# Kernel optimization log

Hardware: AMD Instinct MI355X
Metric: run time of the kernel (lower is better)

Reference implementation:

```python
import jax, jax.numpy as jnp
import numpy as np

N = 25000        # nodes
E = 400000       # edges (avg 16 neighbors)
C1 = 8           # output_size (scalar channels into TP)
COUT = 16        # channels_out
LMAX = 2
NB = 8           # number_of_basis
RMAX = 5.0       # max_radius
EMB = 16         # atom embedding dim
NATOM = 10
WNUM = (LMAX + 1) * C1 * COUT                 # per-edge TP weights (parity-shared, k0 paths)
TOTAL_DIM = 2 * COUT * (1 + 3 + 9)            # both parities x ranks 0..2 -> 416


def setup_inputs() -> dict:
    key = jax.random.key(0)
    ks = jax.random.split(key, 12)
    rn = lambda i, shape, s=1.0: jax.random.normal(ks[i], shape, jnp.float32) * s
    pos = rn(0, (N, 3)) * 3.0
    A = jax.random.randint(ks[1], (N,), 0, NATOM)
    batch = jnp.zeros((N,), jnp.int32)                       # single graph
    edge_src = jax.random.randint(ks[2], (E,), 0, N)
    # avoid self-edges (zero-length vectors)
    edge_dst = (edge_src + jax.random.randint(ks[3], (E,), 1, N)) % N
    edge_shifts = jnp.zeros((E, 3), jnp.float32)
    cell = jnp.eye(3, dtype=jnp.float32)[None] * 10.0        # [1,3,3]
    emb_table = rn(4, (NATOM, EMB))
    atom_w1 = rn(5, (EMB, 64), EMB ** -0.5)
    atom_b1 = jnp.zeros((64,), jnp.float32)
    atom_w2 = rn(6, (64, C1), 64 ** -0.5)
    atom_b2 = jnp.zeros((C1,), jnp.float32)
    fc_w1 = rn(7, (NB, 64), NB ** -0.5)
    fc_b1 = jnp.zeros((64,), jnp.float32)
    fc_w2 = rn(8, (64, 64), 64 ** -0.5)
    fc_b2 = jnp.zeros((64,), jnp.float32)
    fc_w3 = rn(9, (64, WNUM), 64 ** -0.5)
    fc_b3 = jnp.zeros((WNUM,), jnp.float32)
    return dict(pos=pos, A=A, batch=batch, edge_src=edge_src, edge_dst=edge_dst,
                edge_shifts=edge_shifts, cell=cell, emb_table=emb_table,
                atom_w1=atom_w1, atom_b1=atom_b1, atom_w2=atom_w2, atom_b2=atom_b2,
                fc_w1=fc_w1, fc_b1=fc_b1, fc_w2=fc_w2, fc_b2=fc_b2, fc_w3=fc_w3, fc_b3=fc_b3)


def reference(pos, A, batch, edge_src, edge_dst, edge_shifts, cell, emb_table,
              atom_w1, atom_b1, atom_w2, atom_b2,
              fc_w1, fc_b1, fc_w2, fc_b2, fc_w3, fc_b3):
    num_edges = edge_src.shape[0]
    num_nodes = pos.shape[0]
    # edge geometry (PBC shift)
    edge_cells = cell[batch[edge_src]]                                   # [E,3,3]
    shift_vecs = jnp.einsum('ni,nij->nj', edge_shifts, edge_cells)
    edge_vec = pos[edge_dst] - pos[edge_src] + shift_vecs                # [E,3]
    edge_length = jnp.sqrt(jnp.sum(edge_vec * edge_vec, axis=1) + 1e-12)
    # per-node scalar features -> gathered to edges
    Ai = jax.nn.silu(emb_table[A] @ atom_w1 + atom_b1) @ atom_w2 + atom_b2  # [N,C1]
    Ai_e = Ai[edge_src]                                                    # [E,C1]
    # edge_rank_powers (normalized): rank-0 scalar 1, rank-1 u, rank-2 u\otimes u
    u = edge_vec / edge_length[:, None]
    # radial basis: e3nn soft_one_hot_linspace (gaussian, cutoff) * sqrt(NB)
    values = jnp.linspace(0.0, RMAX, NB + 2)[1:-1]
    step = RMAX / (NB + 1)
    diff = (edge_length[:, None] - values) / step
    emb = (jnp.exp(-diff * diff) / 1.12) * (NB ** 0.5)                     # [E,NB]
    # radial MLP -> per-edge TP weights
    h = jax.nn.silu(emb @ fc_w1 + fc_b1)
    h = jax.nn.silu(h @ fc_w2 + fc_b2)
    w = (h @ fc_w3 + fc_b3).reshape(num_edges, LMAX + 1, C1, COUT)
    # sparse cartesian O(3) tensor product (k0 paths; only (0,0)x(0,L)->(0,L) nonzero
    # since all x1 L>=1 and parity-1 blocks are zero by construction)
    b0 = jnp.einsum('eco,ec->eo', w[:, 0], Ai_e)                           # [E,COUT]
    b1 = jnp.einsum('eco,ec,ei->eoi', w[:, 1], Ai_e, u)                    # [E,COUT,3]
    b2 = jnp.einsum('eco,ec,ei,ej->eoij', w[:, 2], Ai_e, u, u)             # [E,COUT,3,3]
    feats = jnp.concatenate([b0, b1.reshape(num_edges, -1), b2.reshape(num_edges, -1)], axis=1)
    edge_features = jnp.concatenate([feats, jnp.zeros_like(feats)], axis=1)  # pseudo blocks = 0
    # scatter-sum to destination nodes, normalize by global avg num neighbors
    out = jax.ops.segment_sum(edge_features, edge_dst, num_segments=num_nodes)
    avg_num_neighbors = jnp.maximum(jnp.float32(num_edges) / jnp.float32(num_nodes), 1e-8)
    return out / avg_num_neighbors
```

## Files before the change

### kernel.cpp

```cpp
#include <hip/hip_runtime.h>
#include <math.h>

#define NN 25000
#define NE 400000
#define TD 416
#define TCAP 46080
#define NROWS (TCAP * 10)
#define PLH 64
#define NCAP 64
#define GROWS 32
#define BPT (TCAP / 64)

typedef __attribute__((ext_vector_type(8))) __bf16 bf16x8;
typedef __attribute__((ext_vector_type(4))) _Float16 f16x4;
typedef __attribute__((ext_vector_type(4))) float f32x4;

__device__ __forceinline__ float silu_f(float x) {
    return x * __builtin_amdgcn_rcpf(1.0f + __expf(-x));
}

__global__ __launch_bounds__(256) void prep_count_k(
    const float* __restrict__ emb_table,
    const float* __restrict__ aw1, const float* __restrict__ ab1,
    const float* __restrict__ aw2, const float* __restrict__ ab2,
    const float* __restrict__ fw1, const float* __restrict__ fb1,
    const float* __restrict__ fw2,
    const float* __restrict__ fw3, const float* __restrict__ fb3,
    __bf16* __restrict__ w1a, __bf16* __restrict__ w2a,
    __bf16* __restrict__ w3ta, float* __restrict__ b3t,
    const int* __restrict__ esrc, const int* __restrict__ edst,
    const int* __restrict__ A,
    const float* __restrict__ pos, const float* __restrict__ shifts,
    const float* __restrict__ cell, const int* __restrict__ batch,
    int* __restrict__ cnt_dst, int* __restrict__ cnt_t,
    int4* __restrict__ tlist4) {
    const int tid = threadIdx.x;
    if (blockIdx.x < 64) {
        __shared__ float s_ai[80];
        if (tid < 10) {
            float acc[8];
#pragma unroll
            for (int o = 0; o < 8; ++o) acc[o] = ab2[o];
            for (int j = 0; j < 64; ++j) {
                float h = ab1[j];
#pragma unroll
                for (int i = 0; i < 16; ++i) h += emb_table[tid * 16 + i] * aw1[i * 64 + j];
                h = silu_f(h);
#pragma unroll
                for (int o = 0; o < 8; ++o) acc[o] += h * aw2[j * 8 + o];
            }
#pragma unroll
            for (int o = 0; o < 8; ++o) s_ai[tid * 8 + o] = acc[o];
        }
        __syncthreads();
        for (int i = blockIdx.x * 256 + tid; i < 37344; i += 64 * 256) {
            if (i < 2048) {
                int m = i >> 9, r = i & 511, lane = r >> 3, j = r & 7;
                int k = (lane >> 4) * 8 + j, ch = m * 16 + (lane & 15);
                float v = (k < 8) ? fw1[k * 64 + ch] : ((k == 8) ? fb1[ch] : 0.0f);
                w1a[i] = (__bf16)v;
            } else if (i < 6144) {
                int q = i - 2048;
                int mk = q >> 9, lane = (q >> 3) & 63, j = q & 7;
                int m = mk >> 1, kt = mk & 1;
                int k = kt * 32 + (lane >> 4) * 8 + j, ch = m * 16 + (lane & 15);
                w2a[q] = (__bf16)fw2[k * 64 + ch];
            } else if (i < 36864) {
                int q = i - 6144;
                int tmk = q >> 9, lane = (q >> 3) & 63, j = q & 7;
                int kt = tmk & 1, tm = tmk >> 1;
                int t = tm / 3, m = tm - t * 3;
                int k = kt * 32 + (lane >> 4) * 8 + j, ch = m * 16 + (lane & 15);
                int l = ch >> 4, o = ch & 15;
                float s = 0.f;
#pragma unroll
                for (int c = 0; c < 8; ++c)
                    s += s_ai[t * 8 + c] * fw3[k * 384 + l * 128 + c * 16 + o];
                w3ta[q] = (__bf16)s;
            } else {
                int q2 = i - 36864;
                int t = q2 / 48, ch = q2 - t * 48;
                int l = ch >> 4, o = ch & 15;
                float s = 0.f;
#pragma unroll
                for (int c = 0; c < 8; ++c)
                    s += s_ai[t * 8 + c] * fb3[l * 128 + c * 16 + o];
                b3t[q2] = s;
            }
        }
    } else {
        __shared__ int lcnt[10];
        __shared__ int gbase[10];
        if (tid < 10) lcnt[tid] = 0;
        __syncthreads();
        int e = (blockIdx.x - 64) * 256 + tid;
        int t = 0, lr = 0;
        int4 rec;
        bool valid = e < NE;
        if (valid) {
            const int dst = edst[e];
            const int src = esrc[e];
            int rank = atomicAdd(&cnt_dst[dst], 1);
            t = A[src];
            lr = atomicAdd(&lcnt[t], 1);
            const int b = batch[src];
            const float* cb = cell + b * 9;
            const float sh0 = shifts[e * 3 + 0], sh1 = shifts[e * 3 + 1], sh2 = shifts[e * 3 + 2];
            float vx = pos[dst * 3 + 0] - pos[src * 3 + 0] + sh0 * cb[0] + sh1 * cb[3] + sh2 * cb[6];
            float vy = pos[dst * 3 + 1] - pos[src * 3 + 1] + sh0 * cb[1] + sh1 * cb[4] + sh2 * cb[7];
            float vz = pos[dst * 3 + 2] - pos[src * 3 + 2] + sh0 * cb[2] + sh1 * cb[5] + sh2 * cb[8];
            rec.x = __float_as_int(vx);
            rec.y = __float_as_int(vy);
            rec.z = __float_as_int(vz);
            rec.w = (dst << 6) | rank;
        }
        __syncthreads();
        if (tid < 10) gbase[tid] = atomicAdd(&cnt_t[tid], lcnt[tid]);
        __syncthreads();
        if (valid) tlist4[t * TCAP + gbase[t] + lr] = rec;
    }
}

__global__ __launch_bounds__(64) void edge_k(
    const int4* __restrict__ tlist4, const int* __restrict__ cnt_t,
    const __bf16* __restrict__ w1a, const __bf16* __restrict__ w2a,
    const __bf16* __restrict__ w3ta,
    const float* __restrict__ fb2, const float* __restrict__ b3t,
    _Float16* __restrict__ payload) {
    __shared__ __bf16 embuf[64 * 8];
    __shared__ __bf16 h1buf[16 * 72];
    __shared__ __bf16 h2buf[16 * 72];
    __shared__ int pbuf[64];
    const int lane = threadIdx.x;
    const int t_blk = blockIdx.x / BPT;
    const int local = (blockIdx.x - t_blk * BPT) * 64;
    const int nval = cnt_t[t_blk];
    if (local >= nval) return;

    const int idx = min(local + lane, nval - 1);
    const int4 rec = tlist4[t_blk * TCAP + idx];
    const float vx = __int_as_float(rec.x);
    const float vy = __int_as_float(rec.y);
    const float vz = __int_as_float(rec.z);
    const int pd = rec.w;
    pbuf[lane] = pd;

    const float l2 = vx * vx + vy * vy + vz * vz + 1e-12f;
    const float il = __builtin_amdgcn_rsqf(l2);
    const float len = l2 * il;
    {
        const uint4 z4 = {0u, 0u, 0u, 0u};
        union { float f[4]; uint4 u; } uu;
        uu.f[0] = vx * il; uu.f[1] = vy * il; uu.f[2] = vz * il; uu.f[3] = 0.f;
        *(uint4*)(payload + (size_t)pd * PLH + 48) = uu.u;
        *(uint4*)(payload + (size_t)pd * PLH + 56) = z4;
    }

    bf16x8 er0;
#pragma unroll
    for (int k = 0; k < 8; ++k) {
        float d = (len - (5.0f * (float)(k + 1) / 9.0f)) * 1.8f;
        er0[k] = (__bf16)(__expf(-d * d) * 2.525381361380528f);
    }
    *(bf16x8*)&embuf[lane * 8] = er0;

    bf16x8 a1[4], a2[8], a3[6];
#pragma unroll
    for (int m = 0; m < 4; ++m) a1[m] = *(const bf16x8*)(w1a + (m * 64 + lane) * 8);
#pragma unroll
    for (int i = 0; i < 8; ++i) a2[i] = *(const bf16x8*)(w2a + (i * 64 + lane) * 8);
#pragma unroll
    for (int i = 0; i < 6; ++i)
        a3[i] = *(const bf16x8*)(w3ta + ((size_t)(t_blk * 6 + i) * 64 + lane) * 8);
    const int q = lane >> 4;
    const int qr = q * 4;
    const int q8 = q * 8;
    const int colrow = lane & 15;
    f32x4 bias2[4], bias3[3];
#pragma unroll
    for (int m = 0; m < 4; ++m) bias2[m] = *(const f32x4*)(fb2 + m * 16 + qr);
#pragma unroll
    for (int m = 0; m < 3; ++m) bias3[m] = *(const f32x4*)(b3t + t_blk * 48 + m * 16 + qr);

    bf16x8 bone = {};
    bone[0] = (__bf16)1.0f;
    __syncthreads();

    const float SC = (float)NN / (float)NE;
#pragma unroll 1
    for (int n = 0; n < 4; ++n) {
        const int erow = n * 16 + colrow;
        bf16x8 bd = *(bf16x8*)&embuf[erow * 8];
        bf16x8 b1 = (q == 0) ? bd : bone;
#pragma unroll
        for (int m = 0; m < 4; ++m) {
            f32x4 c = {0.f, 0.f, 0.f, 0.f};
            c = __builtin_amdgcn_mfma_f32_16x16x32_bf16(a1[m], b1, c, 0, 0, 0);
            __bf16 hp[4];
#pragma unroll
            for (int r = 0; r < 4; ++r) hp[r] = (__bf16)silu_f(c[r]);
            *(uint2*)&h1buf[colrow * 72 + m * 16 + qr] = *(uint2*)hp;
        }
        __syncthreads();
        bf16x8 b20 = *(bf16x8*)&h1buf[colrow * 72 + q8];
        bf16x8 b21 = *(bf16x8*)&h1buf[colrow * 72 + 32 + q8];
#pragma unroll
        for (int m = 0; m < 4; ++m) {
            f32x4 c = bias2[m];
            c = __builtin_amdgcn_mfma_f32_16x16x32_bf16(a2[m * 2 + 0], b20, c, 0, 0, 0);
            c = __builtin_amdgcn_mfma_f32_16x16x32_bf16(a2[m * 2 + 1], b21, c, 0, 0, 0);
            __bf16 hp[4];
#pragma unroll
            for (int r = 0; r < 4; ++r) hp[r] = (__bf16)silu_f(c[r]);
            *(uint2*)&h2buf[colrow * 72 + m * 16 + qr] = *(uint2*)hp;
        }
        __syncthreads();
        const int prow = pbuf[erow];
        bf16x8 b30 = *(bf16x8*)&h2buf[colrow * 72 + q8];
        bf16x8 b31 = *(bf16x8*)&h2buf[colrow * 72 + 32 + q8];
#pragma unroll
        for (int m = 0; m < 3; ++m) {
            f32x4 c = bias3[m];
            c = __builtin_amdgcn_mfma_f32_16x16x32_bf16(a3[m * 2 + 0], b30, c, 0, 0, 0);
            c = __builtin_amdgcn_mfma_f32_16x16x32_bf16(a3[m * 2 + 1], b31, c, 0, 0, 0);
            f16x4 hp;
#pragma unroll
            for (int r = 0; r < 4; ++r) hp[r] = (_Float16)(c[r] * SC);
            *(f16x4*)(payload + (size_t)prow * PLH + m * 16 + qr) = hp;
        }
    }
}

__global__ __launch_bounds__(256) void gather_k(const int* __restrict__ cnt_dst,
                                                const _Float16* __restrict__ payload,
                                                float* __restrict__ out) {
    __shared__ __align__(16) _Float16 sp_s[GROWS][72];
    __shared__ float sfac[GROWS][16];
    const int n = blockIdx.x;
    const int tid = threadIdx.x;
    const int lo = n * NCAP;
    const int cnt = cnt_dst[n];
    int voff = 0, foff = 0;
    if (tid < 16) { voff = tid; foff = 0; }
    else if (tid < 64) { int q = tid - 16; voff = 16 + q / 3; foff = 1 + q % 3; }
    else if (tid < 208) { int q = tid - 64; voff = 32 + q / 9; foff = 4 + q % 9; }
    float acc = 0.f;
    for (int p0 = 0; p0 < cnt; p0 += GROWS) {
        const int m = min(GROWS, cnt - p0);
        if (tid < m * 8) {
            int r = tid >> 3, q = tid & 7;
            ((uint4*)&sp_s[r][0])[q] = ((const uint4*)(payload + (size_t)(lo + p0 + r) * PLH))[q];
        }
        __syncthreads();
        for (int idx = tid; idx < m * 16; idx += 256) {
            int r = idx >> 4, f = idx & 15;
            if (f < 13) {
                const float* uf = (const float*)&sp_s[r][48];
                float v;
                if (f == 0) v = 1.0f;
                else if (f < 4) v = uf[f - 1];
                else { int g = f - 4; v = uf[g / 3] * uf[g % 3]; }
                sfac[r][f] = v;
            }
        }
        __syncthreads();
        if (tid < 208)
            for (int r = 0; r < m; ++r)
                acc += (float)sp_s[r][voff] * sfac[r][foff];
        __syncthreads();
    }
    if (tid < 208) {
        out[(size_t)n * TD + tid] = acc;
        out[(size_t)n * TD + 208 + tid] = 0.f;
    }
}

extern "C" void kernel_launch(void* const* d_in, const int* in_sizes, int n_in,
                              void* d_out, int out_size, void* d_ws, size_t ws_size,
                              hipStream_t stream) {
    const float* pos       = (const float*)d_in[0];
    const int*   A         = (const int*)d_in[1];
    const int*   batch     = (const int*)d_in[2];
    const int*   esrc      = (const int*)d_in[3];
    const int*   edst      = (const int*)d_in[4];
    const float* shifts    = (const float*)d_in[5];
    const float* cell      = (const float*)d_in[6];
    const float* emb_table = (const float*)d_in[7];
    const float* aw1       = (const float*)d_in[8];
    const float* ab1       = (const float*)d_in[9];
    const float* aw2       = (const float*)d_in[10];
    const float* ab2       = (const float*)d_in[11];
    const float* fw1       = (const float*)d_in[12];
    const float* fb1       = (const float*)d_in[13];
    const float* fw2       = (const float*)d_in[14];
    const float* fb2       = (const float*)d_in[15];
    const float* fw3       = (const float*)d_in[16];
    const float* fb3       = (const float*)d_in[17];
    float* out = (float*)d_out;

    char* base = (char*)d_ws;
    __bf16* w1a    = (__bf16*)(base + 0);
    __bf16* w2a    = (__bf16*)(base + 4096);
    __bf16* w3ta   = (__bf16*)(base + 12288);
    float*  b3t    = (float*)(base + 73728);
    int* cnt_dst   = (int*)(base + 75648);
    int* cnt_t     = (int*)(base + 175680);
    int4* tlist4   = (int4*)(base + 175808);
    _Float16* payload = (_Float16*)(base + 7548672);

    hipMemsetAsync(cnt_dst, 0, 100160, stream);
    prep_count_k<<<64 + (NE + 255) / 256, 256, 0, stream>>>(
        emb_table, aw1, ab1, aw2, ab2, fw1, fb1, fw2, fw3, fb3,
        w1a, w2a, w3ta, b3t, esrc, edst, A, pos, shifts, cell, batch,
        cnt_dst, cnt_t, tlist4);
    edge_k<<<10 * BPT, 64, 0, stream>>>(tlist4, cnt_t, w1a, w2a, w3ta, fb2, b3t, payload);
    gather_k<<<NN, 256, 0, stream>>>(cnt_dst, payload, out);
}
```

Before: 180.5 us.

## Pack multiple waves per block in edge and gather kernels with wave-local sync

```diff
diff --git a/kernel.cpp b/kernel.cpp
--- a/kernel.cpp
+++ b/kernel.cpp
@@ -10,6 +10,8 @@
 #define NCAP 64
 #define GROWS 32
 #define BPT (TCAP / 64)
+#define GPB 4
+#define GW 4
 
 typedef __attribute__((ext_vector_type(8))) __bf16 bf16x8;
 typedef __attribute__((ext_vector_type(4))) _Float16 f16x4;
@@ -17,6 +19,12 @@
 
 __device__ __forceinline__ float silu_f(float x) {
     return x * __builtin_amdgcn_rcpf(1.0f + __expf(-x));
+}
+
+__device__ __forceinline__ void wave_fence() {
+    asm volatile("" ::: "memory");
+    __builtin_amdgcn_wave_barrier();
+    asm volatile("" ::: "memory");
 }
 
 __global__ __launch_bounds__(256) void prep_count_k(
@@ -121,19 +129,20 @@
     }
 }
 
-__global__ __launch_bounds__(64) void edge_k(
+__global__ __launch_bounds__(256) void edge_k(
     const int4* __restrict__ tlist4, const int* __restrict__ cnt_t,
     const __bf16* __restrict__ w1a, const __bf16* __restrict__ w2a,
     const __bf16* __restrict__ w3ta,
     const float* __restrict__ fb2, const float* __restrict__ b3t,
     _Float16* __restrict__ payload) {
-    __shared__ __bf16 embuf[64 * 8];
-    __shared__ __bf16 h1buf[16 * 72];
-    __shared__ __bf16 h2buf[16 * 72];
-    __shared__ int pbuf[64];
-    const int lane = threadIdx.x;
-    const int t_blk = blockIdx.x / BPT;
-    const int local = (blockIdx.x - t_blk * BPT) * 64;
+    __shared__ __bf16 embuf[GPB][64 * 8];
+    __shared__ __bf16 h1buf[GPB][16 * 72];
+    __shared__ __bf16 h2buf[GPB][16 * 72];
+    const int tid = threadIdx.x;
+    const int wid = tid >> 6, lane = tid & 63;
+    const int g = blockIdx.x * GPB + wid;
+    const int t_blk = g / BPT;
+    const int local = (g - t_blk * BPT) * 64;
     const int nval = cnt_t[t_blk];
     if (local >= nval) return;
 
@@ -143,7 +152,6 @@
     const float vy = __int_as_float(rec.y);
     const float vz = __int_as_float(rec.z);
     const int pd = rec.w;
-    pbuf[lane] = pd;
 
     const float l2 = vx * vx + vy * vy + vz * vz + 1e-12f;
     const float il = __builtin_amdgcn_rsqf(l2);
@@ -162,7 +170,7 @@
         float d = (len - (5.0f * (float)(k + 1) / 9.0f)) * 1.8f;
         er0[k] = (__bf16)(__expf(-d * d) * 2.525381361380528f);
     }
-    *(bf16x8*)&embuf[lane * 8] = er0;
+    *(bf16x8*)&embuf[wid][lane * 8] = er0;
 
     bf16x8 a1[4], a2[8], a3[6];
 #pragma unroll
@@ -184,13 +192,13 @@
 
     bf16x8 bone = {};
     bone[0] = (__bf16)1.0f;
-    __syncthreads();
+    wave_fence();
 
     const float SC = (float)NN / (float)NE;
 #pragma unroll 1
     for (int n = 0; n < 4; ++n) {
         const int erow = n * 16 + colrow;
-        bf16x8 bd = *(bf16x8*)&embuf[erow * 8];
+        bf16x8 bd = *(bf16x8*)&embuf[wid][erow * 8];
         bf16x8 b1 = (q == 0) ? bd : bone;
 #pragma unroll
         for (int m = 0; m < 4; ++m) {
@@ -199,11 +207,11 @@
             __bf16 hp[4];
 #pragma unroll
             for (int r = 0; r < 4; ++r) hp[r] = (__bf16)silu_f(c[r]);
-            *(uint2*)&h1buf[colrow * 72 + m * 16 + qr] = *(uint2*)hp;
-        }
-        __syncthreads();
-        bf16x8 b20 = *(bf16x8*)&h1buf[colrow * 72 + q8];
-        bf16x8 b21 = *(bf16x8*)&h1buf[colrow * 72 + 32 + q8];
+            *(uint2*)&h1buf[wid][colrow * 72 + m * 16 + qr] = *(uint2*)hp;
+        }
+        wave_fence();
+        bf16x8 b20 = *(bf16x8*)&h1buf[wid][colrow * 72 + q8];
+        bf16x8 b21 = *(bf16x8*)&h1buf[wid][colrow * 72 + 32 + q8];
 #pragma unroll
         for (int m = 0; m < 4; ++m) {
             f32x4 c = bias2[m];
@@ -212,12 +220,12 @@
             __bf16 hp[4];
 #pragma unroll
             for (int r = 0; r < 4; ++r) hp[r] = (__bf16)silu_f(c[r]);
-            *(uint2*)&h2buf[colrow * 72 + m * 16 + qr] = *(uint2*)hp;
-        }
-        __syncthreads();
-        const int prow = pbuf[erow];
-        bf16x8 b30 = *(bf16x8*)&h2buf[colrow * 72 + q8];
-        bf16x8 b31 = *(bf16x8*)&h2buf[colrow * 72 + 32 + q8];
+            *(uint2*)&h2buf[wid][colrow * 72 + m * 16 + qr] = *(uint2*)hp;
+        }
+        wave_fence();
+        const int prow = __shfl(pd, erow);
+        bf16x8 b30 = *(bf16x8*)&h2buf[wid][colrow * 72 + q8];
+        bf16x8 b31 = *(bf16x8*)&h2buf[wid][colrow * 72 + 32 + q8];
 #pragma unroll
         for (int m = 0; m < 3; ++m) {
             f32x4 c = bias3[m];
@@ -228,50 +236,60 @@
             for (int r = 0; r < 4; ++r) hp[r] = (_Float16)(c[r] * SC);
             *(f16x4*)(payload + (size_t)prow * PLH + m * 16 + qr) = hp;
         }
+        wave_fence();
     }
 }
 
 __global__ __launch_bounds__(256) void gather_k(const int* __restrict__ cnt_dst,
                                                 const _Float16* __restrict__ payload,
                                                 float* __restrict__ out) {
-    __shared__ __align__(16) _Float16 sp_s[GROWS][72];
-    __shared__ float sfac[GROWS][16];
-    const int n = blockIdx.x;
+    __shared__ __align__(16) _Float16 sp[GW][GROWS][80];
     const int tid = threadIdx.x;
-    const int lo = n * NCAP;
+    const int wid = tid >> 6, lane = tid & 63;
+    const int n = blockIdx.x * GW + wid;
+    if (n >= NN) return;
     const int cnt = cnt_dst[n];
-    int voff = 0, foff = 0;
-    if (tid < 16) { voff = tid; foff = 0; }
-    else if (tid < 64) { int q = tid - 16; voff = 16 + q / 3; foff = 1 + q % 3; }
-    else if (tid < 208) { int q = tid - 64; voff = 32 + q / 9; foff = 4 + q % 9; }
-    float acc = 0.f;
+    const size_t lo = (size_t)n * NCAP;
+
+    int voff[4], ia[4], ib[4];
+#pragma unroll
+    for (int j = 0; j < 4; ++j) {
+        int e = lane + 64 * j;
+        int vo = 0, a = 0, bsel = 0;
+        if (e < 16) { vo = e; }
+        else if (e < 64) { int qq = e - 16; vo = 16 + qq / 3; a = 1 + qq % 3; }
+        else if (e < 208) { int qq = e - 64; vo = 32 + qq / 9; int g2 = qq % 9; a = 1 + g2 / 3; bsel = 1 + g2 % 3; }
+        voff[j] = vo; ia[j] = a; ib[j] = bsel;
+    }
+    float acc[4] = {0.f, 0.f, 0.f, 0.f};
+
     for (int p0 = 0; p0 < cnt; p0 += GROWS) {
         const int m = min(GROWS, cnt - p0);
-        if (tid < m * 8) {
-            int r = tid >> 3, q = tid & 7;
-            ((uint4*)&sp_s[r][0])[q] = ((const uint4*)(payload + (size_t)(lo + p0 + r) * PLH))[q];
-        }
-        __syncthreads();
-        for (int idx = tid; idx < m * 16; idx += 256) {
-            int r = idx >> 4, f = idx & 15;
-            if (f < 13) {
-                const float* uf = (const float*)&sp_s[r][48];
-                float v;
-                if (f == 0) v = 1.0f;
-                else if (f < 4) v = uf[f - 1];
-                else { int g = f - 4; v = uf[g / 3] * uf[g % 3]; }
-                sfac[r][f] = v;
+        for (int i = lane; i < m * 8; i += 64) {
+            int r = i >> 3, qq = i & 7;
+            ((uint4*)&sp[wid][r][0])[qq] = ((const uint4*)(payload + (lo + p0 + r) * PLH))[qq];
+        }
+        wave_fence();
+#pragma unroll 1
+        for (int r = 0; r < m; ++r) {
+            const float* uf = (const float*)&sp[wid][r][48];
+            const float u0 = uf[0], u1 = uf[1], u2 = uf[2];
+#pragma unroll
+            for (int j = 0; j < 4; ++j) {
+                float wa = (ia[j] == 0) ? 1.f : ((ia[j] == 1) ? u0 : ((ia[j] == 2) ? u1 : u2));
+                float wb = (ib[j] == 0) ? 1.f : ((ib[j] == 1) ? u0 : ((ib[j] == 2) ? u1 : u2));
+                acc[j] += (float)sp[wid][r][voff[j]] * (wa * wb);
             }
         }
-        __syncthreads();
-        if (tid < 208)
-            for (int r = 0; r < m; ++r)
-                acc += (float)sp_s[r][voff] * sfac[r][foff];
-        __syncthreads();
-    }
-    if (tid < 208) {
-        out[(size_t)n * TD + tid] = acc;
-        out[(size_t)n * TD + 208 + tid] = 0.f;
+        wave_fence();
+    }
+#pragma unroll
+    for (int j = 0; j < 4; ++j) {
+        int e = lane + 64 * j;
+        if (e < 208) {
+            out[(size_t)n * TD + e] = acc[j];
+            out[(size_t)n * TD + 208 + e] = 0.f;
+        }
     }
 }
 
@@ -313,6 +331,6 @@
         emb_table, aw1, ab1, aw2, ab2, fw1, fb1, fw2, fw3, fb3,
         w1a, w2a, w3ta, b3t, esrc, edst, A, pos, shifts, cell, batch,
         cnt_dst, cnt_t, tlist4);
-    edge_k<<<10 * BPT, 64, 0, stream>>>(tlist4, cnt_t, w1a, w2a, w3ta, fb2, b3t, payload);
-    gather_k<<<NN, 256, 0, stream>>>(cnt_dst, payload, out);
-}
+    edge_k<<<10 * BPT / GPB, 256, 0, stream>>>(tlist4, cnt_t, w1a, w2a, w3ta, fb2, b3t, payload);
+    gather_k<<<(NN + GW - 1) / GW, 256, 0, stream>>>(cnt_dst, payload, out);
+}
```

Result: slower. 190.6 us (+5.6%).
